# Kernel optimization log

Measured on AMD Instinct MI355X. Metric: run time of the kernel, lower is better.

Reference implementation:

```python
import jax, jax.numpy as jnp
import numpy as np

K = 3  # == stride, neighbors per token


def setup_inputs() -> dict:
    key = jax.random.key(0)
    k1, k2, k3 = jax.random.split(key, 3)
    x = jax.random.normal(k1, (16, 64, 2048), dtype=jnp.float32)        # (B, C, T)
    W = jax.random.normal(k2, (64, 64, K), dtype=jnp.float32) * 0.05     # (O, I, K) conv1d weight
    b = jax.random.normal(k3, (64,), dtype=jnp.float32) * 0.05           # (O,) conv1d bias
    return {"x": x, "W": W, "b": b}


def reference(x, W, b):
    B, C, T = x.shape
    # pairwise squared euclidean distances over the channel dim: (B, T, T)
    nsq = jnp.sum(x * x, axis=1)                       # (B, T)
    dot = jnp.einsum('bct,bcs->bts', x, x)             # (B, T, T)
    dist = jnp.maximum(nsq[:, :, None] + nsq[:, None, :] - 2.0 * dot, 0.0)
    # K nearest neighbors (smallest distance -> top_k of negated dist)
    _, idx = jax.lax.top_k(-dist, K)                   # (B, T, K) int32 indices
    # gather neighbor features: prime[b, c, i*K + k] = x[b, c, idx[b, i, k]]
    idx_flat = idx.reshape(B, 1, T * K)
    prime = jnp.take_along_axis(x, jnp.broadcast_to(idx_flat, (B, C, T * K)), axis=2)
    # Conv1d with kernel_size=K, stride=K, padding=0 -> output length T
    out = jax.lax.conv_general_dilated(
        prime, W, window_strides=(K,), padding='VALID',
        dimension_numbers=('NCH', 'OIH', 'NCH'))
    return out + b[None, :, None]
```

## Files before the change

kernel.cpp:

```cpp
#include <hip/hip_runtime.h>

#define B_ 16
#define C_ 64
#define T_ 2048
#define O_ 64
#define KNN 3
#define HSPLIT 4
#define JCH (T_ / HSPLIT)
#define NJS (JCH / 32)

typedef short short8   __attribute__((ext_vector_type(8)));
typedef float f32x4    __attribute__((ext_vector_type(4)));
typedef unsigned short ushortx4 __attribute__((ext_vector_type(4)));

#define XT_OFF 0
#define XS_OFF (XT_OFF + B_ * T_ * C_)
#define NSQ_OFF (XS_OFF + B_ * T_ * C_)
#define WT_OFF (NSQ_OFF + B_ * T_)
#define CAND_OFF (WT_OFF + 192 * O_)

__device__ inline ushort bf16_rne(float f) {
    union { float f; unsigned u; } cv; cv.f = f;
    unsigned u = cv.u;
    u += 0x7FFF + ((u >> 16) & 1);
    return (ushort)(u >> 16);
}
__device__ inline float bf16_val(ushort h) {
    union { unsigned u; float f; } cv; cv.u = ((unsigned)h) << 16; return cv.f;
}

__global__ __launch_bounds__(256) void prep_kernel(const float* __restrict__ x,
                                                   const float* __restrict__ W,
                                                   float* __restrict__ ws) {
    float*  xT  = ws + XT_OFF;
    ushort* xs  = (ushort*)(ws + XS_OFF);
    float*  nsq = ws + NSQ_OFF;
    float*  Wt  = ws + WT_OFF;
    int blk = blockIdx.x;
    int tid = threadIdx.x;
    if (blk < B_ * (T_ / 64)) {
        int b  = blk / (T_ / 64);
        int t0 = (blk % (T_ / 64)) * 64;
        __shared__ float tl[64 * 65];
        #pragma unroll
        for (int r = 0; r < 16; ++r) {
            int e = r * 256 + tid;
            int c = e >> 6, t = e & 63;
            tl[c * 65 + t] = x[(b * C_ + c) * T_ + t0 + t];
        }
        __syncthreads();
        #pragma unroll
        for (int r = 0; r < 16; ++r) {
            int e = r * 256 + tid;
            int t = e >> 6, c = e & 63;
            float v = tl[c * 65 + t];
            size_t rowg = (size_t)(b * T_ + t0 + t);
            xT[rowg * 64 + c] = v;
            ushort hi = bf16_rne(v);
            float  fr = v - bf16_val(hi);
            ushort lo = bf16_rne(fr);
            xs[rowg * 128 + c]      = hi;
            xs[rowg * 128 + 64 + c] = lo;
        }
        if (tid < 64) {
            float s = 0.f;
            #pragma unroll
            for (int c = 0; c < 64; ++c) { float v = tl[c * 65 + tid]; s = fmaf(v, v, s); }
            nsq[b * T_ + t0 + tid] = s;
        }
    } else {
        int e = (blk - B_ * (T_ / 64)) * 256 + tid;
        if (e < O_ * C_ * KNN) {
            int o = e / (C_ * KNN);
            int c = (e / KNN) % C_;
            int k = e % KNN;
            Wt[(k * 64 + c) * O_ + o] = W[e];
        }
    }
}

__global__ __launch_bounds__(256, 4) void knn_mfma_kernel(const ushort* __restrict__ xs,
                                                          const float* __restrict__ nsq,
                                                          ushort* __restrict__ cand) {
    __shared__ __align__(16) ushort jbuf[4][32 * 128];
    __shared__ float nsqs[JCH];

    int bid = blockIdx.x;
    int g   = bid & 63;
    int m   = bid >> 6;
    int b   = g >> 2, h = g & 3;
    int i0  = m * 128;
    int tid = threadIdx.x;
    int w   = tid >> 6, l = tid & 63, lr = l & 15, lq = l >> 4;
    const ushort* xsb = xs + (size_t)b * T_ * 128;
    int jBase = h * JCH;

    if (tid < JCH / 4)
        ((float4*)nsqs)[tid] = ((const float4*)(nsq + b * T_ + jBase))[tid];

    short8 bA0, bA1, bA4, bA5, bB0, bB1, bB4, bB5;
    {
        const ushort* ia = xsb + (size_t)(i0 + w * 32 + lr) * 128 + lq * 8;
        bA0 = *(const short8*)(ia + 0);  bA1 = *(const short8*)(ia + 32);
        bA4 = *(const short8*)(ia + 64); bA5 = *(const short8*)(ia + 96);
        const ushort* ib2 = ia + 16 * 128;
        bB0 = *(const short8*)(ib2 + 0);  bB1 = *(const short8*)(ib2 + 32);
        bB4 = *(const short8*)(ib2 + 64); bB5 = *(const short8*)(ib2 + 96);
    }
    float niA = nsq[b * T_ + i0 + w * 32 + lr] + 4.0f;
    float niB = nsq[b * T_ + i0 + w * 32 + 16 + lr] + 4.0f;

    const float INF = __builtin_inff();
    float kA0 = INF, kA1 = INF, kA2 = INF, kA3 = INF;
    float kB0 = INF, kB1 = INF, kB2 = INF, kB3 = INF;

    int cSw = lr ^ (w * 4 + lq);
    #define ISSUE_DMA(jsv, bufv) {                                               \
        _Pragma("unroll")                                                        \
        for (int p = 0; p < 2; ++p) {                                            \
            int rloc = p * 16 + w * 4 + lq;                                      \
            const ushort* gp = xsb + (size_t)(jBase + (jsv) * 32 + rloc) * 128 + cSw * 8; \
            __builtin_amdgcn_global_load_lds(                                    \
                (const __attribute__((address_space(1))) void*)gp,               \
                (__attribute__((address_space(3))) void*)(jbuf[bufv] + (p * 16 + w * 4) * 128), \
                16, 0, 0);                                                       \
        } }

    asm volatile("s_waitcnt lgkmcnt(0)" ::: "memory");

    ISSUE_DMA(0, 0);
    ISSUE_DMA(1, 1);
    ISSUE_DMA(2, 2);

    #pragma unroll 1
    for (int js = 0; js < NJS; ++js) {
        if (js <= NJS - 3)      asm volatile("s_waitcnt vmcnt(4)" ::: "memory");
        else if (js == NJS - 2) asm volatile("s_waitcnt vmcnt(2)" ::: "memory");
        else                    asm volatile("s_waitcnt vmcnt(0)" ::: "memory");
        __builtin_amdgcn_s_barrier();
        asm volatile("" ::: "memory");
        __builtin_amdgcn_sched_barrier(0);
        if (js + 3 < NJS) ISSUE_DMA(js + 3, (js + 3) & 3);
        const char* jb8 = (const char*)jbuf[js & 3];
        #pragma unroll
        for (int tile = 0; tile < 2; ++tile) {
            const char* rowp = jb8 + (tile * 16 + lr) * 256;
            short8 ah0 = *(const short8*)(rowp + ((( 0 + lq) ^ lr) << 4));
            short8 ah1 = *(const short8*)(rowp + ((( 4 + lq) ^ lr) << 4));
            short8 al0 = *(const short8*)(rowp + ((( 8 + lq) ^ lr) << 4));
            short8 al1 = *(const short8*)(rowp + (((12 + lq) ^ lr) << 4));
            f32x4 accA = {0.f, 0.f, 0.f, 0.f};
            f32x4 accB = {0.f, 0.f, 0.f, 0.f};
            accA = __builtin_amdgcn_mfma_f32_16x16x32_bf16(ah0, bA0, accA, 0, 0, 0);
            accB = __builtin_amdgcn_mfma_f32_16x16x32_bf16(ah0, bB0, accB, 0, 0, 0);
            accA = __builtin_amdgcn_mfma_f32_16x16x32_bf16(ah1, bA1, accA, 0, 0, 0);
            accB = __builtin_amdgcn_mfma_f32_16x16x32_bf16(ah1, bB1, accB, 0, 0, 0);
            accA = __builtin_amdgcn_mfma_f32_16x16x32_bf16(al0, bA0, accA, 0, 0, 0);
            accB = __builtin_amdgcn_mfma_f32_16x16x32_bf16(al0, bB0, accB, 0, 0, 0);
            accA = __builtin_amdgcn_mfma_f32_16x16x32_bf16(al1, bA1, accA, 0, 0, 0);
            accB = __builtin_amdgcn_mfma_f32_16x16x32_bf16(al1, bB1, accB, 0, 0, 0);
            accA = __builtin_amdgcn_mfma_f32_16x16x32_bf16(ah0, bA4, accA, 0, 0, 0);
            accB = __builtin_amdgcn_mfma_f32_16x16x32_bf16(ah0, bB4, accB, 0, 0, 0);
            accA = __builtin_amdgcn_mfma_f32_16x16x32_bf16(ah1, bA5, accA, 0, 0, 0);
            accB = __builtin_amdgcn_mfma_f32_16x16x32_bf16(ah1, bB5, accB, 0, 0, 0);
            float4 nv = *(const float4*)(nsqs + js * 32 + tile * 16 + lq * 4);
            int idb = ((js * 2 + tile) << 2) | (lq << 8);
            #define INS(K0, K1, K2, K3, sv, idv) {                                  \
                unsigned uu = (__float_as_uint(sv) & 0xFFFFFC00u) | (unsigned)(idv); \
                float kf = __uint_as_float(uu);                                      \
                float n0 = fminf(K0, kf);                                            \
                float n1 = __builtin_amdgcn_fmed3f(K0, K1, kf);                      \
                float n2 = __builtin_amdgcn_fmed3f(K1, K2, kf);                      \
                float n3 = __builtin_amdgcn_fmed3f(K2, K3, kf);                      \
                K0 = n0; K1 = n1; K2 = n2; K3 = n3; }
            {
                float s0 = fmaf(-2.f, accA[0], nv.x + niA); INS(kA0, kA1, kA2, kA3, s0, idb + 0);
                float s1 = fmaf(-2.f, accA[1], nv.y + niA); INS(kA0, kA1, kA2, kA3, s1, idb + 1);
                float s2 = fmaf(-2.f, accA[2], nv.z + niA); INS(kA0, kA1, kA2, kA3, s2, idb + 2);
                float s3 = fmaf(-2.f, accA[3], nv.w + niA); INS(kA0, kA1, kA2, kA3, s3, idb + 3);
            }
            {
                float s0 = fmaf(-2.f, accB[0], nv.x + niB); INS(kB0, kB1, kB2, kB3, s0, idb + 0);
                float s1 = fmaf(-2.f, accB[1], nv.y + niB); INS(kB0, kB1, kB2, kB3, s1, idb + 1);
                float s2 = fmaf(-2.f, accB[2], nv.z + niB); INS(kB0, kB1, kB2, kB3, s2, idb + 2);
                float s3 = fmaf(-2.f, accB[3], nv.w + niB); INS(kB0, kB1, kB2, kB3, s3, idb + 3);
            }
            #undef INS
        }
    }

    __syncthreads();
    float* fbuf = (float*)jbuf;
    {
        float* pa = fbuf + (w * 32 + lr) * 16 + lq * 4;
        pa[0] = kA0; pa[1] = kA1; pa[2] = kA2; pa[3] = kA3;
        float* pb = fbuf + (w * 32 + 16 + lr) * 16 + lq * 4;
        pb[0] = kB0; pb[1] = kB1; pb[2] = kB2; pb[3] = kB3;
    }
    __syncthreads();
    if (l < 32) {
        int rloc = w * 32 + l;
        const float* pr = fbuf + rloc * 16;
        float m0 = INF, m1 = INF, m2 = INF, m3 = INF;
        #pragma unroll
        for (int q2 = 0; q2 < 16; ++q2) {
            float kf = pr[q2];
            float n0 = fminf(m0, kf);
            float n1 = __builtin_amdgcn_fmed3f(m0, m1, kf);
            float n2 = __builtin_amdgcn_fmed3f(m1, m2, kf);
            float n3 = __builtin_amdgcn_fmed3f(m2, m3, kf);
            m0 = n0; m1 = n1; m2 = n2; m3 = n3;
        }
        ushortx4 cv;
        #define DEC(mf, slot) { unsigned u = __float_as_uint(mf) & 1023u;            \
            cv[slot] = (ushort)(jBase + (((u >> 2) & 63u) << 4) + ((u >> 8) << 2) + (u & 3)); }
        DEC(m0, 0); DEC(m1, 1); DEC(m2, 2); DEC(m3, 3);
        #undef DEC
        int row = b * T_ + i0 + rloc;
        *(ushortx4*)(cand + (size_t)row * 16 + h * 4) = cv;
    }
}

__global__ __launch_bounds__(256, 4) void conv_fused_kernel(const float* __restrict__ ws,
                                                            const float* __restrict__ bias,
                                                            float* __restrict__ out) {
    const float*  xT   = ws + XT_OFF;
    const float*  nsq  = ws + NSQ_OFF;
    const float*  Wt   = ws + WT_OFF;
    const ushort* cand = (const ushort*)(ws + CAND_OFF);

    __shared__ float g_s[192 * 32];
    __shared__ int   jsel3[32 * 3];

    int bb  = blockIdx.x >> 6;
    int i0  = (blockIdx.x & 63) * 32;
    int tid = threadIdx.x;
    int w = tid >> 6, l = tid & 63, qw = l >> 4, lr = l & 15;
    int bT = bb * T_;

    const float INF = __builtin_inff();
    #pragma unroll
    for (int it = 0; it < 2; ++it) {
        int rl  = w * 8 + it * 4 + qw;
        int row = bT + i0 + rl;
        float4 av = *(const float4*)(xT + (size_t)row * 64 + lr * 4);
        int jown = cand[(size_t)row * 16 + lr];
        float D0 = INF, D1 = INF, D2 = INF;
        int   I0 = 0x7FFFFFFF, I1 = 0x7FFFFFFF, I2 = 0x7FFFFFFF;
        #pragma unroll
        for (int t = 0; t < 16; ++t) {
            int jt = __shfl(jown, (l & 48) + t, 64);
            float4 bv = *(const float4*)(xT + (size_t)(bT + jt) * 64 + lr * 4);
            float p = fmaf(bv.w, av.w, fmaf(bv.z, av.z, fmaf(bv.y, av.y, bv.x * av.x)));
            p += __shfl_xor(p, 1, 64);
            p += __shfl_xor(p, 2, 64);
            p += __shfl_xor(p, 4, 64);
            p += __shfl_xor(p, 8, 64);
            float s = nsq[bT + jt] - 2.f * p;
            bool lt2 = (s < D2) || (s == D2 && jt < I2);
            bool lt1 = (s < D1) || (s == D1 && jt < I1);
            bool lt0 = (s < D0) || (s == D0 && jt < I0);
            float nD2 = lt1 ? D1 : (lt2 ? s : D2); int nI2 = lt1 ? I1 : (lt2 ? jt : I2);
            float nD1 = lt0 ? D0 : (lt1 ? s : D1); int nI1 = lt0 ? I0 : (lt1 ? jt : I1);
            D2 = nD2; I2 = nI2; D1 = nD1; I1 = nI1;
            D0 = lt0 ? s : D0; I0 = lt0 ? jt : I0;
        }
        if (lr == 0) {
            jsel3[rl * 3 + 0] = I0; jsel3[rl * 3 + 1] = I1; jsel3[rl * 3 + 2] = I2;
        }
    }
    __syncthreads();

    if (tid < 96) {
        int k  = tid >> 5;
        int ip = tid & 31;
        int j  = jsel3[ip * 3 + k];
        const float4* src = (const float4*)(xT + (size_t)(bT + j) * 64);
        #pragma unroll
        for (int c4 = 0; c4 < 16; ++c4) {
            float4 v = src[c4];
            int mm = k * 64 + c4 * 4;
            g_s[(mm + 0) * 32 + ip] = v.x;
            g_s[(mm + 1) * 32 + ip] = v.y;
            g_s[(mm + 2) * 32 + ip] = v.z;
            g_s[(mm + 3) * 32 + ip] = v.w;
        }
    }
    __syncthreads();

    int oq = tid >> 4;
    int iq = tid & 15;
    float a0x = 0.f, a0y = 0.f, a1x = 0.f, a1y = 0.f;
    float a2x = 0.f, a2y = 0.f, a3x = 0.f, a3y = 0.f;
    #pragma unroll 4
    for (int mm = 0; mm < 192; ++mm) {
        float4 wv = *(const float4*)(Wt + mm * 64 + oq * 4);
        float2 gv = *(const float2*)(g_s + mm * 32 + iq * 2);
        a0x = fmaf(wv.x, gv.x, a0x); a0y = fmaf(wv.x, gv.y, a0y);
        a1x = fmaf(wv.y, gv.x, a1x); a1y = fmaf(wv.y, gv.y, a1y);
        a2x = fmaf(wv.z, gv.x, a2x); a2y = fmaf(wv.z, gv.y, a2y);
        a3x = fmaf(wv.w, gv.x, a3x); a3y = fmaf(wv.w, gv.y, a3y);
    }
    int o0 = oq * 4;
    float b0 = bias[o0], b1 = bias[o0 + 1], b2 = bias[o0 + 2], b3 = bias[o0 + 3];
    float2 r0; r0.x = a0x + b0; r0.y = a0y + b0;
    float2 r1; r1.x = a1x + b1; r1.y = a1y + b1;
    float2 r2; r2.x = a2x + b2; r2.y = a2y + b2;
    float2 r3; r3.x = a3x + b3; r3.y = a3y + b3;
    size_t ob = (size_t)(bb * O_ + o0) * T_ + i0 + iq * 2;
    *(float2*)(out + ob)          = r0;
    *(float2*)(out + ob + T_)     = r1;
    *(float2*)(out + ob + 2 * T_) = r2;
    *(float2*)(out + ob + 3 * T_) = r3;
}

extern "C" void kernel_launch(void* const* d_in, const int* in_sizes, int n_in,
                              void* d_out, int out_size, void* d_ws, size_t ws_size,
                              hipStream_t stream) {
    const float* x    = (const float*)d_in[0];
    const float* W    = (const float*)d_in[1];
    const float* bias = (const float*)d_in[2];
    float* out = (float*)d_out;
    float* ws  = (float*)d_ws;

    prep_kernel<<<B_ * (T_ / 64) + 48, 256, 0, stream>>>(x, W, ws);
    knn_mfma_kernel<<<1024, 256, 0, stream>>>(
        (const ushort*)(ws + XS_OFF), ws + NSQ_OFF, (ushort*)(ws + CAND_OFF));
    conv_fused_kernel<<<B_ * 64, 256, 0, stream>>>(ws, bias, out);
}
```

Measured before the change: 146.3 us.

## Remap block indices by batch and restructure candidate rerank and gather parallelism

Both kernels now decode the block index so that consecutive blocks cover eight different batches, which changes cache locality and the scheduling order. In the conv kernel, each group of 4 lanes computes one candidate's full 64-channel dot product, so the shuffle reduction needs 2 steps instead of 4. The distances and indices are written to shared memory that aliases g_s, and a single thread per row then does the serial top-3 selection. The neighbour gather now uses 192 threads, each loading half a row, instead of 96 threads loading a full row. The cost is an extra barrier, and only 32 threads are active during the top-3 selection.

```diff
diff --git a/kernel.cpp b/kernel.cpp
--- a/kernel.cpp
+++ b/kernel.cpp
@@ -86,9 +86,9 @@
     __shared__ float nsqs[JCH];
 
     int bid = blockIdx.x;
-    int g   = bid & 63;
-    int m   = bid >> 6;
-    int b   = g >> 2, h = g & 3;
+    int b   = (bid & 7) + 8 * (bid >> 9);
+    int h   = (bid >> 3) & 3;
+    int m   = (bid >> 5) & 15;
     int i0  = m * 128;
     int tid = threadIdx.x;
     int w   = tid >> 6, l = tid & 63, lr = l & 15, lq = l >> 4;
@@ -232,31 +232,49 @@
     __shared__ float g_s[192 * 32];
     __shared__ int   jsel3[32 * 3];
 
-    int bb  = blockIdx.x >> 6;
-    int i0  = (blockIdx.x & 63) * 32;
+    float* sref = g_s;
+    int*   jref = (int*)(g_s + 32 * 17);
+
+    int bid = blockIdx.x;
+    int bb  = (bid & 7) + 8 * (bid >> 9);
+    int i0  = ((bid >> 3) & 63) * 32;
     int tid = threadIdx.x;
-    int w = tid >> 6, l = tid & 63, qw = l >> 4, lr = l & 15;
+    int w = tid >> 6, l = tid & 63;
     int bT = bb * T_;
 
     const float INF = __builtin_inff();
-    #pragma unroll
-    for (int it = 0; it < 2; ++it) {
-        int rl  = w * 8 + it * 4 + qw;
+    int cd  = l >> 2;
+    int c16 = l & 3;
+    #pragma unroll 2
+    for (int rr = 0; rr < 8; ++rr) {
+        int rl  = w * 8 + rr;
         int row = bT + i0 + rl;
-        float4 av = *(const float4*)(xT + (size_t)row * 64 + lr * 4);
-        int jown = cand[(size_t)row * 16 + lr];
+        int jt  = cand[(size_t)row * 16 + cd];
+        const float4* bvp = (const float4*)(xT + (size_t)(bT + jt) * 64 + c16 * 16);
+        const float4* avp = (const float4*)(xT + (size_t)row * 64 + c16 * 16);
+        float4 b0 = bvp[0], b1 = bvp[1], b2 = bvp[2], b3 = bvp[3];
+        float4 a0 = avp[0], a1 = avp[1], a2 = avp[2], a3 = avp[3];
+        float p0 = fmaf(b0.w, a0.w, fmaf(b0.z, a0.z, fmaf(b0.y, a0.y, b0.x * a0.x)));
+        float p1 = fmaf(b1.w, a1.w, fmaf(b1.z, a1.z, fmaf(b1.y, a1.y, b1.x * a1.x)));
+        float p2 = fmaf(b2.w, a2.w, fmaf(b2.z, a2.z, fmaf(b2.y, a2.y, b2.x * a2.x)));
+        float p3 = fmaf(b3.w, a3.w, fmaf(b3.z, a3.z, fmaf(b3.y, a3.y, b3.x * a3.x)));
+        float p = (p0 + p1) + (p2 + p3);
+        p += __shfl_xor(p, 1, 64);
+        p += __shfl_xor(p, 2, 64);
+        float s = nsq[bT + jt] - 2.f * p;
+        if (c16 == 0) { sref[rl * 17 + cd] = s; jref[rl * 17 + cd] = jt; }
+    }
+    __syncthreads();
+
+    if (tid < 32) {
+        const float* sp = sref + tid * 17;
+        const int*   jp = jref + tid * 17;
         float D0 = INF, D1 = INF, D2 = INF;
         int   I0 = 0x7FFFFFFF, I1 = 0x7FFFFFFF, I2 = 0x7FFFFFFF;
         #pragma unroll
         for (int t = 0; t < 16; ++t) {
-            int jt = __shfl(jown, (l & 48) + t, 64);
-            float4 bv = *(const float4*)(xT + (size_t)(bT + jt) * 64 + lr * 4);
-            float p = fmaf(bv.w, av.w, fmaf(bv.z, av.z, fmaf(bv.y, av.y, bv.x * av.x)));
-            p += __shfl_xor(p, 1, 64);
-            p += __shfl_xor(p, 2, 64);
-            p += __shfl_xor(p, 4, 64);
-            p += __shfl_xor(p, 8, 64);
-            float s = nsq[bT + jt] - 2.f * p;
+            float s  = sp[t];
+            int   jt = jp[t];
             bool lt2 = (s < D2) || (s == D2 && jt < I2);
             bool lt1 = (s < D1) || (s == D1 && jt < I1);
             bool lt0 = (s < D0) || (s == D0 && jt < I0);
@@ -265,21 +283,21 @@
             D2 = nD2; I2 = nI2; D1 = nD1; I1 = nI1;
             D0 = lt0 ? s : D0; I0 = lt0 ? jt : I0;
         }
-        if (lr == 0) {
-            jsel3[rl * 3 + 0] = I0; jsel3[rl * 3 + 1] = I1; jsel3[rl * 3 + 2] = I2;
-        }
-    }
-    __syncthreads();
-
-    if (tid < 96) {
-        int k  = tid >> 5;
-        int ip = tid & 31;
-        int j  = jsel3[ip * 3 + k];
-        const float4* src = (const float4*)(xT + (size_t)(bT + j) * 64);
-        #pragma unroll
-        for (int c4 = 0; c4 < 16; ++c4) {
-            float4 v = src[c4];
-            int mm = k * 64 + c4 * 4;
+        jsel3[tid * 3 + 0] = I0; jsel3[tid * 3 + 1] = I1; jsel3[tid * 3 + 2] = I2;
+    }
+    __syncthreads();
+
+    if (tid < 192) {
+        int k    = tid >> 6;
+        int r6   = tid & 63;
+        int ip   = r6 >> 1;
+        int half = r6 & 1;
+        int j = jsel3[ip * 3 + k];
+        const float4* src = (const float4*)(xT + (size_t)(bT + j) * 64 + half * 32);
+        #pragma unroll
+        for (int q = 0; q < 8; ++q) {
+            float4 v = src[q];
+            int mm = k * 64 + (half * 8 + q) * 4;
             g_s[(mm + 0) * 32 + ip] = v.x;
             g_s[(mm + 1) * 32 + ip] = v.y;
             g_s[(mm + 2) * 32 + ip] = v.z;
```

After: 143.5 us. Within noise of the previous version (-1.9%).
